# Performance work log

Measured on AMD Instinct MI355X. Metric: run time of the kernel, lower is better.

The kernel has to match this reference:

```python
import jax, jax.numpy as jnp
import numpy as np

N, E, NG = 8192, 65536, 8
EMB, SH = 32, 9
HID = EMB * SH
SDIM, M, KV = 16, 2048, 16  # M = master_rate*N masters (static top-k); KV virtual nbrs/node
RMAX, NB, PC = 10.0, 8, 5
MLPD, MSH, NL = 64, 32, 3
NEMB = 10


def _radial(r):
    # r: [E,1] -> Bessel basis * polynomial cutoff envelope, [E, NB]
    x = r / RMAX
    n = jnp.arange(1, NB + 1, dtype=r.dtype)
    bes = jnp.sqrt(2.0 / RMAX) * jnp.sin(n * jnp.pi * x) / jnp.maximum(r, 1e-9)
    p = float(PC)
    env = (1.0 - (p + 1) * (p + 2) / 2 * x ** PC + p * (p + 2) * x ** (PC + 1)
           - p * (p + 1) / 2 * x ** (PC + 2))
    env = jnp.where(x < 1.0, env, 0.0)
    return bes * env


def _sph(vec):
    # component-normalized real spherical harmonics l=0,1,2 of normalized vec
    r = jnp.linalg.norm(vec, axis=-1, keepdims=True)
    u = vec / jnp.maximum(r, 1e-9)
    x, y, z = u[..., 0], u[..., 1], u[..., 2]
    s3, s5, s15 = jnp.sqrt(3.0), jnp.sqrt(5.0), jnp.sqrt(15.0)
    Y = jnp.stack([
        jnp.ones_like(x),
        s3 * y, s3 * z, s3 * x,
        s15 * x * y, s15 * y * z, 0.5 * s5 * (3 * z * z - 1.0),
        s15 * x * z, 0.5 * s15 * (x * x - y * y)], axis=-1)
    return Y, r


def _conv(h, src, dst, sh, ef, W, rw1, rb1, rw2, rb2, valid, nnodes):
    # TFN-style conv: per-edge radial MLP -> per-sh-path weights, tensor product, scatter-sum
    rad = jax.nn.relu(ef @ rw1 + rb1) @ rw2 + rb2  # [E, SH]
    coeff = sh * rad                               # [E, SH]
    h_src = h[src]                                 # gather [E, in]
    out = W.shape[-1]
    msg = jnp.zeros((src.shape[0], out), h.dtype)
    for s in range(SH):  # small fixed loop over sh paths (avoids [E,in*SH] blowup)
        msg = msg + coeff[:, s:s + 1] * (h_src @ W[:, s, :])
    if valid is not None:
        msg = msg * valid[:, None]
    return jnp.zeros((nnodes, out), h.dtype).at[dst].add(msg)


def _scatter_softmax(sc, idx, nseg):
    mx = jax.ops.segment_max(sc, idx, nseg)
    e = jnp.exp(sc - mx[idx])
    s = jax.ops.segment_sum(e, idx, nseg)
    return e / (s[idx] + 1e-9)


def _forward(atoms, pos, edge_index, batch_ids, emb_table, W0, W12,
             rw1, rb1, rw2, rb2, msw1, msb1, msw2, msb2,
             vq, vk, aw1, ab1, aw2, ab2, pw1, pb1, pw2, pb2):
    h = emb_table[atoms]
    src, dst = edge_index[0], edge_index[1]
    for i in range(NL):
        W = W0 if i == 0 else W12[i - 1]
        # ---- local message passing over original edges ----
        vec = pos[src] - pos[dst]
        sh, r = _sph(vec)
        ef = _radial(r)
        h_up = _conv(h, src, dst, sh, ef, W, rw1[i], rb1[i], rw2[i], rb2[i], None, N)
        h_local = h_up.at[:, :h.shape[-1]].add(h)  # h_update + right-pad(h)
        # ---- master selection (static top-k of soft scores, k = master_rate*N) ----
        hs = h_local[:, :SDIM]
        m = jax.nn.sigmoid((jax.nn.relu(hs @ msw1[i] + msb1[i]) @ msw2[i] + msb2[i])[:, 0])
        _, midx = jax.lax.top_k(m, M)
        midx = jnp.sort(midx)
        inv = jnp.full((N,), -1, jnp.int32).at[midx].set(jnp.arange(M, dtype=jnp.int32))
        ms, md = inv[src], inv[dst]
        vi = (ms >= 0) & (md >= 0)           # induced-subgraph edge mask
        msc = jnp.where(vi, ms, 0)
        mdc = jnp.where(vi, md, 0)
        vif = vi.astype(h.dtype)
        h_m = h_local[midx]
        pos_m = pos[midx]
        hms = h_m[:, :SDIM]
        # induced dense adjacency over masters
        adj = jnp.minimum(jnp.zeros((M, M), h.dtype).at[msc, mdc].add(vif), 1.0)
        # ---- virtual edge generation (attention over masters) ----
        S = (hms @ vq[i]) @ (hms @ vk[i]).T / jnp.sqrt(jnp.asarray(SDIM, h.dtype))
        blocked = jnp.eye(M, dtype=bool) | (adj > 0)
        S = jnp.where(blocked, -jnp.inf, S)
        A_virtual = jax.nn.softmax(S, axis=-1)
        _, tk = jax.lax.top_k(S, KV)          # top-KV virtual nbrs per master (static)
        row = jnp.repeat(jnp.arange(M), KV)
        col = tk.reshape(-1)
        sv = jnp.concatenate([row, col])      # undirected virtual edges
        dv = jnp.concatenate([col, row])
        # ---- master-level edges: induced (masked) + virtual ----
        srcm = jnp.concatenate([msc, sv])
        dstm = jnp.concatenate([mdc, dv])
        vecm = pos_m[srcm] - pos_m[dstm]
        shm, rm = _sph(vecm)
        efm = _radial(rm)
        # scatter-softmax attention weights on virtual edges
        att_in = jnp.concatenate([hms[sv], hms[dv], efm[E:]], axis=-1)
        sc = (jax.nn.relu(att_in @ aw1[i] + ab1[i]) @ aw2[i] + ab2[i])[:, 0]
        wv = _scatter_softmax(sc, dv, M)
        full_w = jnp.concatenate([vif, wv])   # induced edges weight 1 (0 if invalid)
        efm = efm * full_w[:, None]
        if i == 0:
            h_hier = h_m  # first layer: in_irreps != out_irreps -> skip master conv
        else:
            validm = jnp.concatenate([vif, jnp.ones_like(wv)])
            h_mu = _conv(h_m, srcm, dstm, shm, efm, W,
                         rw1[i], rb1[i], rw2[i], rb2[i], validm, M)
            h_hier = h_mu + h_m
        # ---- scatter masters back, soft mix ----
        h_exp = jnp.zeros_like(h_local).at[midx].set(h_hier)
        me = m[:, None]
        h = (1.0 - me) * h_local + me * h_exp
    pooled = jax.ops.segment_sum(h[:, :EMB], batch_ids, NG)  # global_add_pool
    return jax.nn.relu(pooled @ pw1 + pb1) @ pw2 + pb2


def setup_inputs() -> dict:
    key = jax.random.key(0)
    ks = jax.random.split(key, 30)
    g = lambda k, shape, s=0.1: jax.random.normal(k, shape, jnp.float32) * s
    return dict(
        atoms=jax.random.randint(ks[0], (N,), 0, NEMB),
        pos=jax.random.normal(ks[1], (N, 3), jnp.float32) * 3.0,
        edge_index=jax.random.randint(ks[2], (2, E), 0, N),
        batch_ids=jnp.sort(jax.random.randint(ks[3], (N,), 0, NG)),
        emb_table=g(ks[4], (NEMB, EMB), 1.0),
        W0=g(ks[5], (EMB, SH, HID)),
        W12=g(ks[6], (NL - 1, HID, SH, HID), 0.05),
        rw1=g(ks[7], (NL, NB, MLPD), 0.3), rb1=g(ks[8], (NL, MLPD)),
        rw2=g(ks[9], (NL, MLPD, SH), 0.3), rb2=g(ks[10], (NL, SH)),
        msw1=g(ks[11], (NL, SDIM, MSH), 0.3), msb1=g(ks[12], (NL, MSH)),
        msw2=g(ks[13], (NL, MSH, 1), 0.3), msb2=g(ks[14], (NL, 1)),
        vq=g(ks[15], (NL, SDIM, SDIM), 0.3), vk=g(ks[16], (NL, SDIM, SDIM), 0.3),
        aw1=g(ks[17], (NL, 2 * SDIM + NB, SDIM), 0.3), ab1=g(ks[18], (NL, SDIM)),
        aw2=g(ks[19], (NL, SDIM, 1), 0.3), ab2=g(ks[20], (NL, 1)),
        pw1=g(ks[21], (EMB, EMB), 0.3), pb1=g(ks[22], (EMB,)),
        pw2=g(ks[23], (EMB, 1), 0.3), pb2=g(ks[24], (1,)),
    )


def reference(atoms, pos, edge_index, batch_ids, emb_table, W0, W12,
              rw1, rb1, rw2, rb2, msw1, msb1, msw2, msb2,
              vq, vk, aw1, ab1, aw2, ab2, pw1, pb1, pw2, pb2):
    return _forward(atoms, pos, edge_index, batch_ids, emb_table, W0, W12,
                    rw1, rb1, rw2, rb2, msw1, msb1, msw2, msb2,
                    vq, vk, aw1, ab1, aw2, ab2, pw1, pb1, pw2, pb2)
```

## Files before the change

kernel.cpp:

```cpp
#include <hip/hip_runtime.h>
#include <math.h>

#define NN     8192
#define EE     65536
#define NGR    8
#define EMBD   32
#define NSH    9
#define HIDD   288
#define SD     16
#define MM     2048
#define KVK    16
#define NBAS   8
#define MLPDIM 64
#define MSHD   32
#define MK     (MM*KVK)
#define EH     (EE + 2*MK)

typedef __attribute__((ext_vector_type(8))) short bf16x8;
typedef __attribute__((ext_vector_type(4))) float f32x4;

static __device__ __forceinline__ float relu_(float x) { return fmaxf(x, 0.f); }

__device__ __forceinline__ unsigned short f2b(float f) {
  unsigned int u = __float_as_uint(f);
  unsigned int r = (u + 0x7FFFu + ((u >> 16) & 1u)) >> 16;
  return (unsigned short)r;
}
__device__ __forceinline__ float b2f(unsigned short h) {
  return __uint_as_float(((unsigned int)h) << 16);
}

__device__ __forceinline__ void radial8(float r, float ef[8]) {
  float x = r * 0.1f;
  float invr = 1.0f / fmaxf(r, 1e-9f);
  float env = 0.0f;
  if (x < 1.0f) {
    float x2 = x * x, x4 = x2 * x2, x5 = x4 * x;
    env = 1.0f - 21.0f * x5 + 35.0f * x5 * x - 15.0f * x5 * x2;
  }
  const float cst = 0.4472135954999579f;
  float a = 3.14159265358979323846f * x;
#pragma unroll
  for (int n = 1; n <= NBAS; ++n)
    ef[n - 1] = cst * sinf((float)n * a) * invr * env;
}

__device__ __forceinline__ void sph9(float vx, float vy, float vz, float Y[9], float& r) {
  r = sqrtf(vx * vx + vy * vy + vz * vz);
  float inv = 1.0f / fmaxf(r, 1e-9f);
  float x = vx * inv, y = vy * inv, z = vz * inv;
  const float s3 = 1.7320508075688772f, s5 = 2.23606797749979f, s15 = 3.872983346207417f;
  Y[0] = 1.0f;
  Y[1] = s3 * y; Y[2] = s3 * z; Y[3] = s3 * x;
  Y[4] = s15 * x * y; Y[5] = s15 * y * z;
  Y[6] = 0.5f * s5 * (3.0f * z * z - 1.0f);
  Y[7] = s15 * x * z;
  Y[8] = 0.5f * s15 * (x * x - y * y);
}

__device__ __forceinline__ void radmlp(const float ef[8], const float* w1, const float* b1,
                                       const float* w2, const float* b2, float rad[9]) {
  float z[MLPDIM];
#pragma unroll
  for (int d = 0; d < MLPDIM; ++d) {
    float a = b1[d];
#pragma unroll
    for (int b = 0; b < NBAS; ++b) a += ef[b] * w1[b * MLPDIM + d];
    z[d] = relu_(a);
  }
#pragma unroll
  for (int s = 0; s < 9; ++s) {
    float a = b2[s];
#pragma unroll
    for (int d = 0; d < MLPDIM; ++d) a += z[d] * w2[d * 9 + s];
    rad[s] = a;
  }
}

__device__ __forceinline__ unsigned int fkey(float f) {
  unsigned int u = __float_as_uint(f);
  return (u & 0x80000000u) ? ~u : (u | 0x80000000u);
}
__device__ __forceinline__ float funkey(unsigned int k) {
  unsigned int u = (k & 0x80000000u) ? (k ^ 0x80000000u) : ~k;
  return __uint_as_float(u);
}

__device__ __forceinline__ void svdv(int j, const int* __restrict__ tkb, int& s, int& d) {
  if (j < MK) { s = j / KVK; d = tkb[j]; }
  else        { int t = j - MK; s = tkb[t]; d = t / KVK; }
}
__device__ __forceinline__ int dvof(int j, const int* __restrict__ tkb) {
  return (j < MK) ? tkb[j] : (j - MK) / KVK;
}


__global__ void k_init_h(const int* __restrict__ atoms, const float* __restrict__ emb,
                         float* __restrict__ hA) {
  int t = blockIdx.x * 256 + threadIdx.x;
  int n = t / HIDD, c = t - n * HIDD;
  hA[t] = (c < EMBD) ? emb[atoms[n] * EMBD + c] : 0.0f;
}

__global__ void k_geom(const float* __restrict__ pos, const int* __restrict__ ei,
                       float* __restrict__ sh_e, float* __restrict__ ef_e) {
  int e = blockIdx.x * 256 + threadIdx.x;
  int s = ei[e], d = ei[EE + e];
  float vx = pos[s * 3] - pos[d * 3];
  float vy = pos[s * 3 + 1] - pos[d * 3 + 1];
  float vz = pos[s * 3 + 2] - pos[d * 3 + 2];
  float Y[9], r;
  sph9(vx, vy, vz, Y, r);
  float ef[8]; radial8(r, ef);
#pragma unroll
  for (int t = 0; t < 9; ++t) sh_e[e * 9 + t] = Y[t];
#pragma unroll
  for (int b = 0; b < 8; ++b) ef_e[e * 8 + b] = ef[b];
}

__global__ __launch_bounds__(256) void k_radcoeff(const float* __restrict__ ef_e,
    const float* __restrict__ sh_e, const float* __restrict__ rw1, const float* __restrict__ rb1,
    const float* __restrict__ rw2, const float* __restrict__ rb2, float* __restrict__ coeff) {
  __shared__ float w1[NBAS * MLPDIM], b1[MLPDIM], w2[MLPDIM * 9], b2[9];
  int tid = threadIdx.x;
  for (int t = tid; t < NBAS * MLPDIM; t += 256) w1[t] = rw1[t];
  for (int t = tid; t < MLPDIM * 9; t += 256) w2[t] = rw2[t];
  if (tid < MLPDIM) b1[tid] = rb1[tid];
  if (tid < 9) b2[tid] = rb2[tid];
  __syncthreads();
  int e = blockIdx.x * 256 + tid;
  float ef[8];
#pragma unroll
  for (int b = 0; b < 8; ++b) ef[b] = ef_e[e * 8 + b];
  float rad[9]; radmlp(ef, w1, b1, w2, b2, rad);
#pragma unroll
  for (int s = 0; s < 9; ++s) coeff[(size_t)e * 9 + s] = sh_e[e * 9 + s] * rad[s];
}

__global__ __launch_bounds__(256) void k_wt(const float* __restrict__ W, int K,
                                            unsigned short* __restrict__ Whi,
                                            unsigned short* __restrict__ Wlo) {
  __shared__ unsigned short Th[32][290];
  __shared__ unsigned short Tl[32][290];
  int k0 = blockIdx.x * 32;
  int tid = threadIdx.x;
  for (int t = tid; t < 32 * 288; t += 256) {
    int kk = t / 288, o = t % 288;
    float wv = W[(size_t)(k0 + kk) * 288 + o];
    unsigned short hi = f2b(wv);
    Th[kk][o] = hi;
    Tl[kk][o] = f2b(wv - b2f(hi));
  }
  __syncthreads();
  for (int o = tid; o < 288; o += 256) {
    unsigned short th[32], tl[32];
#pragma unroll
    for (int kk = 0; kk < 32; ++kk) { th[kk] = Th[kk][o]; tl[kk] = Tl[kk][o]; }
#pragma unroll
    for (int q = 0; q < 4; ++q) {
      *(float4*)&Whi[(size_t)o * K + k0 + 8 * q] = *(float4*)&th[8 * q];
      *(float4*)&Wlo[(size_t)o * K + k0 + 8 * q] = *(float4*)&tl[8 * q];
    }
  }
}

__global__ void k_hist(const int* __restrict__ didx, int n, int* __restrict__ cnt) {
  int e = blockIdx.x * 256 + threadIdx.x;
  if (e >= n) return;
  int d = didx[e];
  if (d >= 0) atomicAdd(&cnt[d], 1);
}
__global__ __launch_bounds__(256) void k_scan(const int* __restrict__ cnt, int* __restrict__ off,
                                              int* __restrict__ cur, int nb) {
  __shared__ int ps[257];
  int tid = threadIdx.x;
  int chunk = nb / 256;
  int s = 0;
  for (int i = 0; i < chunk; ++i) s += cnt[tid * chunk + i];
  __shared__ int part[256];
  part[tid] = s;
  __syncthreads();
  if (tid == 0) {
    int a = 0;
    for (int i = 0; i < 256; ++i) { ps[i] = a; a += part[i]; }
    ps[256] = a;
  }
  __syncthreads();
  int a = ps[tid];
  for (int i = 0; i < chunk; ++i) {
    int idx = tid * chunk + i;
    off[idx] = a; cur[idx] = a;
    a += cnt[idx];
  }
  if (tid == 255) off[nb] = a;
}
__global__ void k_scat(const int* __restrict__ didx, const int* __restrict__ sidx, int n,
                       int* __restrict__ cur, int* __restrict__ elist, int* __restrict__ esrc) {
  int e = blockIdx.x * 256 + threadIdx.x;
  if (e >= n) return;
  int d = didx[e];
  if (d < 0) return;
  int pos = atomicAdd(&cur[d], 1);
  elist[pos] = e;
  esrc[pos] = sidx[e];
}

template <int NJ>
__global__ __launch_bounds__(256) void k_gatherBbf(const float* __restrict__ h,
    const float* __restrict__ coeff, const int* __restrict__ elist,
    const int* __restrict__ esrc, const int* __restrict__ off,
    unsigned short* __restrict__ Ghi, unsigned short* __restrict__ Glo) {
  constexpr int INW = (NJ == 1) ? 32 : 288;
  constexpr int KG = INW * 9;
  __shared__ float red[3][64][NJ * 9];
  int w = threadIdx.x >> 6, l = threadIdx.x & 63;
  int d = blockIdx.x;
  int e0 = off[d], e1 = off[d + 1];
  float acc[NJ][9];
#pragma unroll
  for (int j = 0; j < NJ; ++j)
#pragma unroll
    for (int s = 0; s < 9; ++s) acc[j][s] = 0.f;
  auto edge = [&](int p) {
    int e = elist[p];
    int src = esrc[p];
    const float* hr = h + (size_t)src * HIDD;
    float hv[NJ];
#pragma unroll
    for (int j = 0; j < NJ; ++j)
      hv[j] = (l + 64 * j < INW) ? hr[l + 64 * j] : 0.f;
    const float* cfp = coeff + (size_t)e * 9;
    float cf[9];
#pragma unroll
    for (int s = 0; s < 9; ++s) cf[s] = cfp[s];
#pragma unroll
    for (int j = 0; j < NJ; ++j)
#pragma unroll
      for (int s = 0; s < 9; ++s) acc[j][s] += hv[j] * cf[s];
  };
  int p = e0 + w;
  for (; p + 4 < e1; p += 8) { edge(p); edge(p + 4); }
  if (p < e1) edge(p);
  if (w > 0) {
#pragma unroll
    for (int j = 0; j < NJ; ++j)
#pragma unroll
      for (int s = 0; s < 9; ++s) red[w - 1][l][j * 9 + s] = acc[j][s];
  }
  __syncthreads();
  if (w == 0) {
#pragma unroll
    for (int j = 0; j < NJ; ++j)
#pragma unroll
      for (int s = 0; s < 9; ++s) {
        int idx = j * 9 + s;
        red[0][l][idx] = acc[j][s] + red[0][l][idx] + red[1][l][idx] + red[2][l][idx];
      }
  }
  __syncthreads();
  unsigned short* Gdh = Ghi + (size_t)d * KG;
  unsigned short* Gdl = Glo + (size_t)d * KG;
  for (int i = threadIdx.x; i < KG; i += 256) {
    int k = i / 9, s = i - 9 * k;
    float v = red[0][k & 63][(k >> 6) * 9 + s];
    unsigned short hi = f2b(v);
    Gdh[i] = hi;
    Gdl[i] = f2b(v - b2f(hi));
  }
}

__global__ __launch_bounds__(256) void k_gatherBf(const float* __restrict__ h,
    const float* __restrict__ coeff, const int* __restrict__ elist,
    const int* __restrict__ esrc, const int* __restrict__ off, float* __restrict__ Gf) {
  constexpr int NJ = 5, INW = 288, KG = 2592, NW = 16;
  __shared__ float red[3][64][NJ * 9];
  int w = threadIdx.x >> 6, l = threadIdx.x & 63;
  int d = blockIdx.x, q = blockIdx.y;
  int e0 = off[d], e1 = off[d + 1];
  float acc[NJ][9];
#pragma unroll
  for (int j = 0; j < NJ; ++j)
#pragma unroll
    for (int s = 0; s < 9; ++s) acc[j][s] = 0.f;
  auto edge = [&](int p) {
    int e = elist[p];
    int src = esrc[p];
    const float* hr = h + (size_t)src * HIDD;
    float hv[NJ];
#pragma unroll
    for (int j = 0; j < NJ; ++j)
      hv[j] = hr[l + 64 * j < INW ? l + 64 * j : 0];
    if (l + 256 >= INW) hv[4] = 0.f;
    const float* cfp = coeff + (size_t)e * 9;
    float cf[9];
#pragma unroll
    for (int s = 0; s < 9; ++s) cf[s] = cfp[s];
#pragma unroll
    for (int j = 0; j < NJ; ++j)
#pragma unroll
      for (int s = 0; s < 9; ++s) acc[j][s] += hv[j] * cf[s];
  };
  int p = e0 + q * 4 + w;
  for (; p + NW < e1; p += 2 * NW) { edge(p); edge(p + NW); }
  if (p < e1) edge(p);
  if (w > 0) {
#pragma unroll
    for (int j = 0; j < NJ; ++j)
#pragma unroll
      for (int s = 0; s < 9; ++s) red[w - 1][l][j * 9 + s] = acc[j][s];
  }
  __syncthreads();
  if (w == 0) {
#pragma unroll
    for (int j = 0; j < NJ; ++j)
#pragma unroll
      for (int s = 0; s < 9; ++s) {
        int idx = j * 9 + s;
        red[0][l][idx] = acc[j][s] + red[0][l][idx] + red[1][l][idx] + red[2][l][idx];
      }
  }
  __syncthreads();
  float* Gd = Gf + ((size_t)q * gridDim.x + d) * KG;
  for (int i = threadIdx.x; i < KG; i += 256) {
    int k = i / 9, s = i - 9 * k;
    Gd[i] = red[0][k & 63][(k >> 6) * 9 + s];
  }
}

__global__ void k_redG(const float* __restrict__ Gf, unsigned short* __restrict__ Ghi,
                       unsigned short* __restrict__ Glo) {
  const size_t PS = (size_t)MM * 2592;
  size_t t = (size_t)blockIdx.x * 256 + threadIdx.x;
  float v = Gf[t] + Gf[PS + t] + Gf[2 * PS + t] + Gf[3 * PS + t];
  unsigned short hi = f2b(v);
  Ghi[t] = hi;
  Glo[t] = f2b(v - b2f(hi));
}

template <int KK>
__global__ __launch_bounds__(256) void k_mgemm3(const unsigned short* __restrict__ Ahi,
    const unsigned short* __restrict__ Alo,
    const unsigned short* __restrict__ Whi, const unsigned short* __restrict__ Wlo,
    float* __restrict__ Cpart) {
  constexpr int slabs = KK / 32;
  __shared__ unsigned short Bh[144 * 40];
  __shared__ unsigned short Bl[144 * 40];
  int m0 = blockIdx.x * 64, cb = blockIdx.y * 144;
  int M = gridDim.x * 64;
  int Z = gridDim.z, z = blockIdx.z;
  int s0 = (z * slabs) / Z, s1 = ((z + 1) * slabs) / Z;
  float* C = Cpart + (size_t)z * M * 288;
  int tid = threadIdx.x;
  int w = tid >> 6, l = tid & 63;
  int lr = l & 15, oct = l >> 4;
  int arow = m0 + 16 * w + lr;
  f32x4 acc[9];
#pragma unroll
  for (int t = 0; t < 9; ++t) acc[t] = (f32x4){0.f, 0.f, 0.f, 0.f};
  for (int sl = s0; sl < s1; ++sl) {
    int k0 = sl * 32;
    __syncthreads();
    for (int t = tid; t < 1152; t += 256) {
      int hsel = t / 576;
      int qq = t - hsel * 576;
      int c = qq >> 2, ko = qq & 3;
      const unsigned short* Wsrc = hsel ? Wlo : Whi;
      float4 v = *(const float4*)&Wsrc[(size_t)(cb + c) * KK + k0 + ko * 8];
      unsigned short* Bdst = hsel ? Bl : Bh;
      *(float4*)&Bdst[c * 40 + ko * 8] = v;
    }
    __syncthreads();
    bf16x8 ah = *(const bf16x8*)&Ahi[(size_t)arow * KK + k0 + oct * 8];
    bf16x8 al = *(const bf16x8*)&Alo[(size_t)arow * KK + k0 + oct * 8];
#pragma unroll
    for (int t = 0; t < 9; ++t) {
      bf16x8 bh = *(const bf16x8*)&Bh[(16 * t + lr) * 40 + oct * 8];
      bf16x8 bl = *(const bf16x8*)&Bl[(16 * t + lr) * 40 + oct * 8];
      acc[t] = __builtin_amdgcn_mfma_f32_16x16x32_bf16(ah, bh, acc[t], 0, 0, 0);
      acc[t] = __builtin_amdgcn_mfma_f32_16x16x32_bf16(ah, bl, acc[t], 0, 0, 0);
      acc[t] = __builtin_amdgcn_mfma_f32_16x16x32_bf16(al, bh, acc[t], 0, 0, 0);
    }
  }
#pragma unroll
  for (int t = 0; t < 9; ++t) {
#pragma unroll
    for (int r = 0; r < 4; ++r)
      C[(size_t)(m0 + 16 * w + 4 * oct + r) * 288 + cb + 16 * t + lr] = acc[t][r];
  }
}

template <int Z>
__global__ void k_redN(const float* __restrict__ part, const float* __restrict__ hA,
                       float* __restrict__ hB, int INL) {
  int t = blockIdx.x * 256 + threadIdx.x;
  float v = 0.f;
#pragma unroll
  for (int z = 0; z < Z; ++z) v += part[(size_t)z * NN * 288 + t];
  int c = t % 288;
  if (c < INL) v += hA[t];
  hB[t] = v;
}
template <int Z>
__global__ void k_redH(const float* __restrict__ part, const float* __restrict__ hM,
                       float* __restrict__ hMu) {
  int t = blockIdx.x * 256 + threadIdx.x;
  float v = hM[t];
#pragma unroll
  for (int z = 0; z < Z; ++z) v += part[(size_t)z * MM * 288 + t];
  hMu[t] = v;
}

__global__ __launch_bounds__(256) void k_mmlp(const float* __restrict__ hB,
    const float* __restrict__ msw1, const float* __restrict__ msb1,
    const float* __restrict__ msw2, const float* __restrict__ msb2, float* __restrict__ mbuf) {
  __shared__ float w1[SD * MSHD], b1[MSHD], w2[MSHD];
  __shared__ float b2s;
  int tid = threadIdx.x;
  for (int t = tid; t < SD * MSHD; t += 256) w1[t] = msw1[t];
  if (tid < MSHD) { b1[tid] = msb1[tid]; w2[tid] = msw2[tid]; }
  if (tid == 0) b2s = msb2[0];
  __syncthreads();
  int n = blockIdx.x * 256 + tid;
  float hs[SD];
#pragma unroll
  for (int k = 0; k < SD; ++k) hs[k] = hB[(size_t)n * HIDD + k];
  float acc = b2s;
#pragma unroll
  for (int d = 0; d < MSHD; ++d) {
    float a = b1[d];
#pragma unroll
    for (int k = 0; k < SD; ++k) a += hs[k] * w1[k * MSHD + d];
    acc += relu_(a) * w2[d];
  }
  mbuf[n] = 1.0f / (1.0f + expf(-acc));
}

__global__ __launch_bounds__(256) void k_rank2(const float* __restrict__ mbuf,
                                               int* __restrict__ rank8) {
  __shared__ float vj[1024];
  __shared__ float vi_s[64];
  __shared__ int part[4][64];
  int tid = threadIdx.x;
  int i0 = blockIdx.x * 64, j0 = blockIdx.y * 1024;
  for (int t = tid; t < 1024; t += 256) vj[t] = mbuf[j0 + t];
  if (tid < 64) vi_s[tid] = mbuf[i0 + tid];
  __syncthreads();
  int il = tid & 63, js = tid >> 6;
  int i = i0 + il;
  float v = vi_s[il];
  int cnt = 0;
#pragma unroll 8
  for (int jj = js * 256; jj < js * 256 + 256; ++jj) {
    float w = vj[jj];
    cnt += (int)((w > v) | ((w == v) & (j0 + jj < i)));
  }
  part[js][il] = cnt;
  __syncthreads();
  if (tid < 64) {
    int c = part[0][tid] + part[1][tid] + part[2][tid] + part[3][tid];
    rank8[(size_t)blockIdx.y * NN + i0 + tid] = c;
  }
}

__global__ __launch_bounds__(256) void k_select2(const int* __restrict__ rank8,
                                                 int* __restrict__ inv, int* __restrict__ midx) {
  __shared__ int part[256], ps[256];
  int tid = threadIdx.x;
  const int CH = NN / 256;
  int base = tid * CH;
  unsigned int mask = 0;
  int s = 0;
#pragma unroll
  for (int i = 0; i < CH; ++i) {
    int r = 0;
#pragma unroll
    for (int y = 0; y < 8; ++y) r += rank8[(size_t)y * NN + base + i];
    int sel = (r < MM) ? 1 : 0;
    mask |= (unsigned int)sel << i;
    s += sel;
  }
  part[tid] = s;
  __syncthreads();
  if (tid == 0) {
    int a = 0;
    for (int i = 0; i < 256; ++i) { ps[i] = a; a += part[i]; }
  }
  __syncthreads();
  int pos = ps[tid];
#pragma unroll
  for (int i = 0; i < CH; ++i) {
    if ((mask >> i) & 1u) {
      inv[base + i] = pos;
      midx[pos] = base + i;
      ++pos;
    } else {
      inv[base + i] = -1;
    }
  }
}

__global__ void k_gather_hm(const float* __restrict__ hB, const int* __restrict__ midx,
                            const float* __restrict__ pos, float* __restrict__ hM,
                            float* __restrict__ posm) {
  int t = blockIdx.x * 256 + threadIdx.x;
  int j = t / HIDD, c = t - j * HIDD;
  int n = midx[j];
  hM[t] = hB[(size_t)n * HIDD + c];
  if (c < 3) posm[j * 3 + c] = pos[n * 3 + c];
}

__global__ void k_qk(const float* __restrict__ hM, const float* __restrict__ vq,
                     const float* __restrict__ vk, float* __restrict__ qb, float* __restrict__ kb) {
  int g = blockIdx.x * 256 + threadIdx.x;
  int j = g >> 5, c = g & 31;
  const float* w = (c < 16) ? vq : vk;
  int cc = c & 15;
  float a = 0.f;
#pragma unroll
  for (int k = 0; k < SD; ++k) a += hM[(size_t)j * HIDD + k] * w[k * SD + cc];
  if (c < 16) qb[j * SD + cc] = a; else kb[j * SD + cc] = a;
}

__global__ __launch_bounds__(256) void k_S(const float* __restrict__ qb,
                                           const float* __restrict__ kb, float* __restrict__ S) {
  __shared__ float qs[64][17], ks[64][17];
  int r0 = blockIdx.y * 64, c0 = blockIdx.x * 64;
  int tid = threadIdx.x;
  for (int t = tid; t < 64 * 16; t += 256) {
    qs[t / 16][t % 16] = qb[(size_t)(r0 + t / 16) * SD + t % 16];
    ks[t / 16][t % 16] = kb[(size_t)(c0 + t / 16) * SD + t % 16];
  }
  __syncthreads();
  int tx = tid & 15, ty = tid >> 4;
  float acc[4][4] = {};
#pragma unroll
  for (int k = 0; k < 16; ++k) {
    float a[4], b[4];
#pragma unroll
    for (int i = 0; i < 4; ++i) a[i] = qs[ty * 4 + i][k];
#pragma unroll
    for (int j = 0; j < 4; ++j) b[j] = ks[tx * 4 + j][k];
#pragma unroll
    for (int i = 0; i < 4; ++i)
#pragma unroll
      for (int j = 0; j < 4; ++j) acc[i][j] += a[i] * b[j];
  }
#pragma unroll
  for (int i = 0; i < 4; ++i)
#pragma unroll
    for (int j = 0; j < 4; ++j) {
      int r = r0 + ty * 4 + i, c = c0 + tx * 4 + j;
      S[(size_t)r * MM + c] = (r == c) ? -INFINITY : acc[i][j] * 0.25f;
    }
}

__global__ void k_adj(const int* __restrict__ ei, const int* __restrict__ inv,
                      float* __restrict__ S) {
  int e = blockIdx.x * 256 + threadIdx.x;
  int ms = inv[ei[e]], md = inv[ei[EE + e]];
  if (ms >= 0 && md >= 0) S[(size_t)ms * MM + md] = -INFINITY;
}

__global__ __launch_bounds__(64) void k_topkv(const float* __restrict__ S, int* __restrict__ tkb) {
  int row = blockIdx.x;
  int lane = threadIdx.x;
  const float* Sr = S + (size_t)row * MM;
  float v[32];
#pragma unroll
  for (int t = 0; t < 32; ++t) v[t] = Sr[lane + 64 * t];
  unsigned int selmask = 0;
  for (int it = 0; it < KVK; ++it) {
    float best = -INFINITY;
    int bcol = 0x7fffffff;
#pragma unroll
    for (int t = 0; t < 32; ++t) {
      if (!((selmask >> t) & 1u)) {
        int c = lane + 64 * t;
        float val = v[t];
        if (val > best || (val == best && c < bcol)) { best = val; bcol = c; }
      }
    }
#pragma unroll
    for (int off = 1; off < 64; off <<= 1) {
      float ov = __shfl_xor(best, off);
      int oc = __shfl_xor(bcol, off);
      if (ov > best || (ov == best && oc < bcol)) { best = ov; bcol = oc; }
    }
    if (lane == (bcol & 63)) selmask |= 1u << (bcol >> 6);
    if (lane == 0) tkb[row * KVK + it] = bcol;
  }
}

__global__ __launch_bounds__(256) void k_att(const float* __restrict__ hM,
    const float* __restrict__ posm, const int* __restrict__ tkb,
    const float* __restrict__ aw1, const float* __restrict__ ab1,
    const float* __restrict__ aw2, const float* __restrict__ ab2, float* __restrict__ scb) {
  __shared__ float w1[40 * SD], b1[SD], w2[SD];
  __shared__ float b2s;
  int tid = threadIdx.x;
  for (int t = tid; t < 40 * SD; t += 256) w1[t] = aw1[t];
  if (tid < SD) { b1[tid] = ab1[tid]; w2[tid] = aw2[tid]; }
  if (tid == 0) b2s = ab2[0];
  __syncthreads();
  int j = blockIdx.x * 256 + tid;
  int s, d; svdv(j, tkb, s, d);
  float vx = posm[s * 3] - posm[d * 3];
  float vy = posm[s * 3 + 1] - posm[d * 3 + 1];
  float vz = posm[s * 3 + 2] - posm[d * 3 + 2];
  float r = sqrtf(vx * vx + vy * vy + vz * vz);
  float ef[8]; radial8(r, ef);
  float hsv[SD], hdv[SD];
  {
    const float4* ps4 = (const float4*)&hM[(size_t)s * HIDD];
    const float4* pd4 = (const float4*)&hM[(size_t)d * HIDD];
#pragma unroll
    for (int q = 0; q < 4; ++q) {
      float4 a = ps4[q], b = pd4[q];
      hsv[4 * q] = a.x; hsv[4 * q + 1] = a.y; hsv[4 * q + 2] = a.z; hsv[4 * q + 3] = a.w;
      hdv[4 * q] = b.x; hdv[4 * q + 1] = b.y; hdv[4 * q + 2] = b.z; hdv[4 * q + 3] = b.w;
    }
  }
  float acc = b2s;
#pragma unroll
  for (int o = 0; o < SD; ++o) {
    float a = b1[o];
#pragma unroll
    for (int k = 0; k < SD; ++k) a += hsv[k] * w1[k * SD + o];
#pragma unroll
    for (int k = 0; k < SD; ++k) a += hdv[k] * w1[(SD + k) * SD + o];
#pragma unroll
    for (int b = 0; b < 8; ++b) a += ef[b] * w1[(2 * SD + b) * SD + o];
    acc += relu_(a) * w2[o];
  }
  scb[j] = acc;
}

__global__ void k_segmax(const float* __restrict__ scb, const int* __restrict__ tkb,
                         unsigned int* __restrict__ segmax) {
  int j = blockIdx.x * 256 + threadIdx.x;
  atomicMax(&segmax[dvof(j, tkb)], fkey(scb[j]));
}
__global__ void k_segexp(const float* __restrict__ scb, const int* __restrict__ tkb,
                         const unsigned int* __restrict__ segmax, float* __restrict__ segsum,
                         float* __restrict__ wvb) {
  int j = blockIdx.x * 256 + threadIdx.x;
  int d = dvof(j, tkb);
  float e = expf(scb[j] - funkey(segmax[d]));
  wvb[j] = e;
  atomicAdd(&segsum[d], e);
}

__global__ void k_hier_first(const int* __restrict__ ei, const int* __restrict__ inv,
                             int* __restrict__ sb, int* __restrict__ db) {
  int e = blockIdx.x * 256 + threadIdx.x;
  int ms = inv[ei[e]], md = inv[ei[EE + e]];
  bool val = (ms >= 0) && (md >= 0);
  sb[e] = val ? ms : 0;
  db[e] = val ? md : -1;
}

__global__ __launch_bounds__(256) void k_coeff_virt(const float* __restrict__ posm,
    const int* __restrict__ tkb, const float* __restrict__ wvb,
    const float* __restrict__ segsum,
    const float* __restrict__ rw1, const float* __restrict__ rb1,
    const float* __restrict__ rw2, const float* __restrict__ rb2,
    float* __restrict__ coeff, int* __restrict__ sb, int* __restrict__ db) {
  __shared__ float w1[NBAS * MLPDIM], b1[MLPDIM], w2[MLPDIM * 9], b2[9];
  int tid = threadIdx.x;
  for (int t = tid; t < NBAS * MLPDIM; t += 256) w1[t] = rw1[t];
  for (int t = tid; t < MLPDIM * 9; t += 256) w2[t] = rw2[t];
  if (tid < MLPDIM) b1[tid] = rb1[tid];
  if (tid < 9) b2[tid] = rb2[tid];
  __syncthreads();
  int j = blockIdx.x * 256 + tid;
  int s, d; svdv(j, tkb, s, d);
  float vx = posm[s * 3] - posm[d * 3];
  float vy = posm[s * 3 + 1] - posm[d * 3 + 1];
  float vz = posm[s * 3 + 2] - posm[d * 3 + 2];
  float Y[9], r;
  sph9(vx, vy, vz, Y, r);
  float ef[8]; radial8(r, ef);
  float w = wvb[j] / (segsum[d] + 1e-9f);
#pragma unroll
  for (int b = 0; b < 8; ++b) ef[b] *= w;
  float rad[9]; radmlp(ef, w1, b1, w2, b2, rad);
  int e = EE + j;
#pragma unroll
  for (int t = 0; t < 9; ++t) coeff[(size_t)e * 9 + t] = Y[t] * rad[t];
  sb[e] = s;
  db[e] = d;
}

__global__ void k_combine(const float* __restrict__ hB, const float* __restrict__ hier,
                          const float* __restrict__ mbuf, const int* __restrict__ inv,
                          float* __restrict__ hA) {
  int t = blockIdx.x * 256 + threadIdx.x;
  int n = t / HIDD;
  float f = mbuf[n];
  float v = (1.0f - f) * hB[t];
  int j = inv[n];
  if (j >= 0) v += f * hier[(size_t)j * HIDD + (t - n * HIDD)];
  hA[t] = v;
}

__global__ __launch_bounds__(256) void k_pool2(const float* __restrict__ hA,
                                               const int* __restrict__ bids,
                                               float* __restrict__ pooled) {
  __shared__ float acc[NGR * EMBD];
  int tid = threadIdx.x;
  acc[tid] = 0.f;
  __syncthreads();
  int c = tid & 31, nloc = tid >> 5;
  int base = blockIdx.x * 256;
  float local = 0.f;
  int curg = -1;
#pragma unroll 4
  for (int k = 0; k < 32; ++k) {
    int n = base + nloc + 8 * k;
    int g = bids[n];
    float v = hA[(size_t)n * HIDD + c];
    if (g != curg) {
      if (curg >= 0) atomicAdd(&acc[curg * EMBD + c], local);
      curg = g; local = 0.f;
    }
    local += v;
  }
  if (curg >= 0) atomicAdd(&acc[curg * EMBD + c], local);
  __syncthreads();
  atomicAdd(&pooled[tid], acc[tid]);
}

__global__ void k_head(const float* __restrict__ pooled, const float* __restrict__ pw1,
                       const float* __restrict__ pb1, const float* __restrict__ pw2,
                       const float* __restrict__ pb2, float* __restrict__ out) {
  __shared__ float z[NGR][EMBD];
  int tid = threadIdx.x;
  int g = tid / EMBD, c2 = tid % EMBD;
  if (g < NGR) {
    float a = pb1[c2];
    for (int c = 0; c < EMBD; ++c) a += pooled[g * EMBD + c] * pw1[c * EMBD + c2];
    z[g][c2] = relu_(a);
  }
  __syncthreads();
  if (tid < NGR) {
    float a = pb2[0];
    for (int c = 0; c < EMBD; ++c) a += z[tid][c] * pw2[c];
    out[tid] = a;
  }
}


extern "C" void kernel_launch(void* const* d_in, const int* in_sizes, int n_in,
                              void* d_out, int out_size, void* d_ws, size_t ws_size,
                              hipStream_t stream) {
  const int* atoms = (const int*)d_in[0];
  const float* pos = (const float*)d_in[1];
  const int* ei = (const int*)d_in[2];
  const int* bids = (const int*)d_in[3];
  const float* emb = (const float*)d_in[4];
  const float* W0 = (const float*)d_in[5];
  const float* W12 = (const float*)d_in[6];
  const float* rw1 = (const float*)d_in[7];
  const float* rb1 = (const float*)d_in[8];
  const float* rw2 = (const float*)d_in[9];
  const float* rb2 = (const float*)d_in[10];
  const float* msw1 = (const float*)d_in[11];
  const float* msb1 = (const float*)d_in[12];
  const float* msw2 = (const float*)d_in[13];
  const float* msb2 = (const float*)d_in[14];
  const float* vq = (const float*)d_in[15];
  const float* vk = (const float*)d_in[16];
  const float* aw1 = (const float*)d_in[17];
  const float* ab1 = (const float*)d_in[18];
  const float* aw2 = (const float*)d_in[19];
  const float* ab2 = (const float*)d_in[20];
  const float* pw1 = (const float*)d_in[21];
  const float* pb1 = (const float*)d_in[22];
  const float* pw2 = (const float*)d_in[23];
  const float* pb2 = (const float*)d_in[24];
  float* out = (float*)d_out;

  char* p = (char*)d_ws;
  auto alloc = [&](size_t n) { char* r = p; p += (n + 255) & ~(size_t)255; return r; };
  float* hA = (float*)alloc((size_t)NN * HIDD * 4);
  float* hB = (float*)alloc((size_t)NN * HIDD * 4);
  float* hM = (float*)alloc((size_t)MM * HIDD * 4);
  float* hMu = (float*)alloc((size_t)MM * HIDD * 4);
  float* S = (float*)alloc((size_t)MM * MM * 4);
  float* sh_e = (float*)alloc((size_t)EE * 9 * 4);
  float* ef_e = (float*)alloc((size_t)EE * 8 * 4);
  float* coeff = (float*)alloc((size_t)EH * 9 * 4);
  float* mbuf = (float*)alloc((size_t)NN * 4);
  int* rank8 = (int*)alloc((size_t)8 * NN * 4);
  int* inv = (int*)alloc((size_t)NN * 4);
  int* midx = (int*)alloc((size_t)MM * 4);
  float* posm = (float*)alloc((size_t)MM * 3 * 4);
  float* qb = (float*)alloc((size_t)MM * SD * 4);
  float* kb = (float*)alloc((size_t)MM * SD * 4);
  int* tkb = (int*)alloc((size_t)MM * KVK * 4);
  float* scb = (float*)alloc((size_t)2 * MK * 4);
  float* wvb = (float*)alloc((size_t)2 * MK * 4);
  unsigned int* segmax = (unsigned int*)alloc((size_t)MM * 4);
  float* segsum = (float*)alloc((size_t)MM * 4);
  int* sb = (int*)alloc((size_t)EH * 4);
  int* db = (int*)alloc((size_t)EH * 4);
  float* pooled = (float*)alloc((size_t)NGR * EMBD * 4);
  char* Gblk = alloc((size_t)NN * 2592 * 4);
  unsigned short* Ghi = (unsigned short*)Gblk;
  unsigned short* Glo = Ghi + (size_t)NN * 2592;
  float* Gf = (float*)Gblk;
  unsigned short* Ghhi = (unsigned short*)alloc((size_t)MM * 2592 * 2);
  unsigned short* Ghlo = (unsigned short*)alloc((size_t)MM * 2592 * 2);
  unsigned short* Wh0 = (unsigned short*)alloc((size_t)288 * 288 * 2);
  unsigned short* Wl0 = (unsigned short*)alloc((size_t)288 * 288 * 2);
  unsigned short* Wh1 = (unsigned short*)alloc((size_t)2592 * 288 * 2);
  unsigned short* Wl1 = (unsigned short*)alloc((size_t)2592 * 288 * 2);
  unsigned short* Wh2 = (unsigned short*)alloc((size_t)2592 * 288 * 2);
  unsigned short* Wl2 = (unsigned short*)alloc((size_t)2592 * 288 * 2);
  float* Cpart = (float*)alloc((size_t)4 * NN * 288 * 4);
  int* cntN = (int*)alloc((size_t)NN * 4);
  int* offN = (int*)alloc((size_t)(NN + 1) * 4);
  int* curN = (int*)alloc((size_t)NN * 4);
  int* elN = (int*)alloc((size_t)EE * 4);
  int* esrcN = (int*)alloc((size_t)EE * 4);
  int* cntH = (int*)alloc((size_t)MM * 4);
  int* offH = (int*)alloc((size_t)(MM + 1) * 4);
  int* curH = (int*)alloc((size_t)MM * 4);
  int* elH = (int*)alloc((size_t)EH * 4);
  int* esrcH = (int*)alloc((size_t)EH * 4);

  const int* srcI = ei;
  const int* dstI = ei + EE;

  k_init_h<<<NN * HIDD / 256, 256, 0, stream>>>(atoms, emb, hA);
  k_geom<<<EE / 256, 256, 0, stream>>>(pos, ei, sh_e, ef_e);

  k_wt<<<288 / 32, 256, 0, stream>>>(W0, 288, Wh0, Wl0);
  k_wt<<<2592 / 32, 256, 0, stream>>>(W12, 2592, Wh1, Wl1);
  k_wt<<<2592 / 32, 256, 0, stream>>>(W12 + (size_t)2592 * 288, 2592, Wh2, Wl2);

  hipMemsetAsync(cntN, 0, NN * 4, stream);
  k_hist<<<EE / 256, 256, 0, stream>>>(dstI, EE, cntN);
  k_scan<<<1, 256, 0, stream>>>(cntN, offN, curN, NN);
  k_scat<<<EE / 256, 256, 0, stream>>>(dstI, srcI, EE, curN, elN, esrcN);

  for (int L = 0; L < 3; ++L) {
    const unsigned short* Wh = (L == 0) ? Wh0 : ((L == 1) ? Wh1 : Wh2);
    const unsigned short* Wl = (L == 0) ? Wl0 : ((L == 1) ? Wl1 : Wl2);
    const float* lrw1 = rw1 + L * NBAS * MLPDIM;
    const float* lrb1 = rb1 + L * MLPDIM;
    const float* lrw2 = rw2 + L * MLPDIM * 9;
    const float* lrb2 = rb2 + L * 9;

    k_radcoeff<<<EE / 256, 256, 0, stream>>>(ef_e, sh_e, lrw1, lrb1, lrw2, lrb2, coeff);
    if (L == 0) {
      k_gatherBbf<1><<<NN, 256, 0, stream>>>(hA, coeff, elN, esrcN, offN, Ghi, Glo);
      k_mgemm3<288><<<dim3(NN / 64, 2, 2), 256, 0, stream>>>(Ghi, Glo, Wh, Wl, Cpart);
      k_redN<2><<<NN * 288 / 256, 256, 0, stream>>>(Cpart, hA, hB, EMBD);
    } else {
      k_gatherBbf<5><<<NN, 256, 0, stream>>>(hA, coeff, elN, esrcN, offN, Ghi, Glo);
      k_mgemm3<2592><<<dim3(NN / 64, 2, 4), 256, 0, stream>>>(Ghi, Glo, Wh, Wl, Cpart);
      k_redN<4><<<NN * 288 / 256, 256, 0, stream>>>(Cpart, hA, hB, HIDD);
    }
    k_mmlp<<<NN / 256, 256, 0, stream>>>(hB, msw1 + L * SD * MSHD, msb1 + L * MSHD,
                                         msw2 + L * MSHD, msb2 + L, mbuf);
    k_rank2<<<dim3(NN / 64, 8), 256, 0, stream>>>(mbuf, rank8);
    k_select2<<<1, 256, 0, stream>>>(rank8, inv, midx);
    k_gather_hm<<<MM * HIDD / 256, 256, 0, stream>>>(hB, midx, pos, hM, posm);

    if (L > 0) {
      k_qk<<<MM * 32 / 256, 256, 0, stream>>>(hM, vq + L * SD * SD, vk + L * SD * SD, qb, kb);
      k_S<<<dim3(MM / 64, MM / 64), 256, 0, stream>>>(qb, kb, S);
      k_adj<<<EE / 256, 256, 0, stream>>>(ei, inv, S);
      k_topkv<<<MM, 64, 0, stream>>>(S, tkb);
      k_att<<<2 * MK / 256, 256, 0, stream>>>(hM, posm, tkb, aw1 + L * 40 * SD, ab1 + L * SD,
                                              aw2 + L * SD, ab2 + L, scb);
      hipMemsetAsync(segmax, 0, 2 * MM * 4, stream);
      k_segmax<<<2 * MK / 256, 256, 0, stream>>>(scb, tkb, segmax);
      k_segexp<<<2 * MK / 256, 256, 0, stream>>>(scb, tkb, segmax, segsum, wvb);
      k_hier_first<<<EE / 256, 256, 0, stream>>>(ei, inv, sb, db);
      k_coeff_virt<<<2 * MK / 256, 256, 0, stream>>>(posm, tkb, wvb, segsum,
                                                     lrw1, lrb1, lrw2, lrb2, coeff, sb, db);
      hipMemsetAsync(cntH, 0, MM * 4, stream);
      k_hist<<<EH / 256, 256, 0, stream>>>(db, EH, cntH);
      k_scan<<<1, 256, 0, stream>>>(cntH, offH, curH, MM);
      k_scat<<<EH / 256, 256, 0, stream>>>(db, sb, EH, curH, elH, esrcH);
      k_gatherBf<<<dim3(MM, 4), 256, 0, stream>>>(hM, coeff, elH, esrcH, offH, Gf);
      k_redG<<<MM * 2592 / 256, 256, 0, stream>>>(Gf, Ghhi, Ghlo);
      k_mgemm3<2592><<<dim3(MM / 64, 2, 8), 256, 0, stream>>>(Ghhi, Ghlo, Wh, Wl, Cpart);
      k_redH<8><<<MM * 288 / 256, 256, 0, stream>>>(Cpart, hM, hMu);
    }
    const float* hier = (L == 0) ? hM : hMu;
    k_combine<<<NN * HIDD / 256, 256, 0, stream>>>(hB, hier, mbuf, inv, hA);
  }

  hipMemsetAsync(pooled, 0, (size_t)NGR * EMBD * 4, stream);
  k_pool2<<<NN / 256, 256, 0, stream>>>(hA, bids, pooled);
  k_head<<<1, 256, 0, stream>>>(pooled, pw1, pb1, pw2, pb2, out);
}
```

Measured before the change: 1.200 ms.

## Enlarge split-bf16 MFMA GEMM tile to 128 rows by full 288 columns

The three-pass bf16 MFMA GEMM now uses 512-thread blocks that each cover 128 rows and all 288 output columns. Each wave computes two 16-row tiles, so every B fragment read from shared memory is used twice, and the whole weight slab is staged once per block instead of being split across two column blocks. The shared-memory padding of 40 is dropped in favour of a dense 32-wide layout. The K-split counts change so the grid stays filled (4 splits for the node GEMMs, 16 for the master GEMM), which adds partial-sum writes and reduction traffic in k_redN and k_redH, and the unpadded layout may cause LDS bank conflicts.

```diff
diff --git a/kernel.cpp b/kernel.cpp
--- a/kernel.cpp
+++ b/kernel.cpp
@@ -338,54 +338,70 @@
 }
 
 template <int KK>
-__global__ __launch_bounds__(256) void k_mgemm3(const unsigned short* __restrict__ Ahi,
+__global__ __launch_bounds__(512) void k_mgemm3(const unsigned short* __restrict__ Ahi,
     const unsigned short* __restrict__ Alo,
     const unsigned short* __restrict__ Whi, const unsigned short* __restrict__ Wlo,
     float* __restrict__ Cpart) {
   constexpr int slabs = KK / 32;
-  __shared__ unsigned short Bh[144 * 40];
-  __shared__ unsigned short Bl[144 * 40];
-  int m0 = blockIdx.x * 64, cb = blockIdx.y * 144;
-  int M = gridDim.x * 64;
-  int Z = gridDim.z, z = blockIdx.z;
+  __shared__ unsigned short Bh[288 * 32];
+  __shared__ unsigned short Bl[288 * 32];
+  int m0 = blockIdx.x * 128;
+  int M = gridDim.x * 128;
+  int Z = gridDim.y, z = blockIdx.y;
   int s0 = (z * slabs) / Z, s1 = ((z + 1) * slabs) / Z;
   float* C = Cpart + (size_t)z * M * 288;
   int tid = threadIdx.x;
   int w = tid >> 6, l = tid & 63;
   int lr = l & 15, oct = l >> 4;
-  int arow = m0 + 16 * w + lr;
-  f32x4 acc[9];
-#pragma unroll
-  for (int t = 0; t < 9; ++t) acc[t] = (f32x4){0.f, 0.f, 0.f, 0.f};
+  int ch = w & 1, rg = w >> 1;
+  int cbase = ch * 144;
+  int ar0 = m0 + rg * 32 + lr;
+  int ar1 = ar0 + 16;
+  f32x4 acc0[9], acc1[9];
+#pragma unroll
+  for (int t = 0; t < 9; ++t) {
+    acc0[t] = (f32x4){0.f, 0.f, 0.f, 0.f};
+    acc1[t] = (f32x4){0.f, 0.f, 0.f, 0.f};
+  }
   for (int sl = s0; sl < s1; ++sl) {
     int k0 = sl * 32;
     __syncthreads();
-    for (int t = tid; t < 1152; t += 256) {
-      int hsel = t / 576;
-      int qq = t - hsel * 576;
+    for (int t = tid; t < 2304; t += 512) {
+      int plane = t / 1152;
+      int qq = t - plane * 1152;
       int c = qq >> 2, ko = qq & 3;
-      const unsigned short* Wsrc = hsel ? Wlo : Whi;
-      float4 v = *(const float4*)&Wsrc[(size_t)(cb + c) * KK + k0 + ko * 8];
-      unsigned short* Bdst = hsel ? Bl : Bh;
-      *(float4*)&Bdst[c * 40 + ko * 8] = v;
+      const unsigned short* Wsrc = plane ? Wlo : Whi;
+      float4 v = *(const float4*)&Wsrc[(size_t)c * KK + k0 + ko * 8];
+      unsigned short* Bdst = plane ? Bl : Bh;
+      *(float4*)&Bdst[qq * 8] = v;
     }
     __syncthreads();
-    bf16x8 ah = *(const bf16x8*)&Ahi[(size_t)arow * KK + k0 + oct * 8];
-    bf16x8 al = *(const bf16x8*)&Alo[(size_t)arow * KK + k0 + oct * 8];
+    bf16x8 ah0 = *(const bf16x8*)&Ahi[(size_t)ar0 * KK + k0 + oct * 8];
+    bf16x8 al0 = *(const bf16x8*)&Alo[(size_t)ar0 * KK + k0 + oct * 8];
+    bf16x8 ah1 = *(const bf16x8*)&Ahi[(size_t)ar1 * KK + k0 + oct * 8];
+    bf16x8 al1 = *(const bf16x8*)&Alo[(size_t)ar1 * KK + k0 + oct * 8];
 #pragma unroll
     for (int t = 0; t < 9; ++t) {
-      bf16x8 bh = *(const bf16x8*)&Bh[(16 * t + lr) * 40 + oct * 8];
-      bf16x8 bl = *(const bf16x8*)&Bl[(16 * t + lr) * 40 + oct * 8];
-      acc[t] = __builtin_amdgcn_mfma_f32_16x16x32_bf16(ah, bh, acc[t], 0, 0, 0);
-      acc[t] = __builtin_amdgcn_mfma_f32_16x16x32_bf16(ah, bl, acc[t], 0, 0, 0);
-      acc[t] = __builtin_amdgcn_mfma_f32_16x16x32_bf16(al, bh, acc[t], 0, 0, 0);
-    }
-  }
+      int idx = (((cbase + 16 * t + lr) << 2) + oct) << 3;
+      bf16x8 bh = *(const bf16x8*)&Bh[idx];
+      bf16x8 bl = *(const bf16x8*)&Bl[idx];
+      acc0[t] = __builtin_amdgcn_mfma_f32_16x16x32_bf16(ah0, bh, acc0[t], 0, 0, 0);
+      acc0[t] = __builtin_amdgcn_mfma_f32_16x16x32_bf16(ah0, bl, acc0[t], 0, 0, 0);
+      acc0[t] = __builtin_amdgcn_mfma_f32_16x16x32_bf16(al0, bh, acc0[t], 0, 0, 0);
+      acc1[t] = __builtin_amdgcn_mfma_f32_16x16x32_bf16(ah1, bh, acc1[t], 0, 0, 0);
+      acc1[t] = __builtin_amdgcn_mfma_f32_16x16x32_bf16(ah1, bl, acc1[t], 0, 0, 0);
+      acc1[t] = __builtin_amdgcn_mfma_f32_16x16x32_bf16(al1, bh, acc1[t], 0, 0, 0);
+    }
+  }
+  int rb0 = m0 + rg * 32 + 4 * oct;
 #pragma unroll
   for (int t = 0; t < 9; ++t) {
-#pragma unroll
-    for (int r = 0; r < 4; ++r)
-      C[(size_t)(m0 + 16 * w + 4 * oct + r) * 288 + cb + 16 * t + lr] = acc[t][r];
+    int cc = cbase + 16 * t + lr;
+#pragma unroll
+    for (int r = 0; r < 4; ++r) {
+      C[(size_t)(rb0 + r) * 288 + cc] = acc0[t][r];
+      C[(size_t)(rb0 + 16 + r) * 288 + cc] = acc1[t][r];
+    }
   }
 }
 
@@ -855,11 +871,11 @@
     k_radcoeff<<<EE / 256, 256, 0, stream>>>(ef_e, sh_e, lrw1, lrb1, lrw2, lrb2, coeff);
     if (L == 0) {
       k_gatherBbf<1><<<NN, 256, 0, stream>>>(hA, coeff, elN, esrcN, offN, Ghi, Glo);
-      k_mgemm3<288><<<dim3(NN / 64, 2, 2), 256, 0, stream>>>(Ghi, Glo, Wh, Wl, Cpart);
-      k_redN<2><<<NN * 288 / 256, 256, 0, stream>>>(Cpart, hA, hB, EMBD);
+      k_mgemm3<288><<<dim3(NN / 128, 4), 512, 0, stream>>>(Ghi, Glo, Wh, Wl, Cpart);
+      k_redN<4><<<NN * 288 / 256, 256, 0, stream>>>(Cpart, hA, hB, EMBD);
     } else {
       k_gatherBbf<5><<<NN, 256, 0, stream>>>(hA, coeff, elN, esrcN, offN, Ghi, Glo);
-      k_mgemm3<2592><<<dim3(NN / 64, 2, 4), 256, 0, stream>>>(Ghi, Glo, Wh, Wl, Cpart);
+      k_mgemm3<2592><<<dim3(NN / 128, 4), 512, 0, stream>>>(Ghi, Glo, Wh, Wl, Cpart);
       k_redN<4><<<NN * 288 / 256, 256, 0, stream>>>(Cpart, hA, hB, HIDD);
     }
     k_mmlp<<<NN / 256, 256, 0, stream>>>(hB, msw1 + L * SD * MSHD, msb1 + L * MSHD,
@@ -887,8 +903,8 @@
       k_scat<<<EH / 256, 256, 0, stream>>>(db, sb, EH, curH, elH, esrcH);
       k_gatherBf<<<dim3(MM, 4), 256, 0, stream>>>(hM, coeff, elH, esrcH, offH, Gf);
       k_redG<<<MM * 2592 / 256, 256, 0, stream>>>(Gf, Ghhi, Ghlo);
-      k_mgemm3<2592><<<dim3(MM / 64, 2, 8), 256, 0, stream>>>(Ghhi, Ghlo, Wh, Wl, Cpart);
-      k_redH<8><<<MM * 288 / 256, 256, 0, stream>>>(Cpart, hM, hMu);
+      k_mgemm3<2592><<<dim3(MM / 128, 16), 512, 0, stream>>>(Ghhi, Ghlo, Wh, Wl, Cpart);
+      k_redH<16><<<MM * 288 / 256, 256, 0, stream>>>(Cpart, hM, hMu);
     }
     const float* hier = (L == 0) ? hM : hMu;
     k_combine<<<NN * HIDD / 256, 256, 0, stream>>>(hB, hier, mbuf, inv, hA);
```

Result: slower. 1.244 ms (+3.6%).
